# Optimization experiments

Hardware: AMD Instinct MI355X
Metric: run time of the kernel (lower is better)

## Reference

```python
import jax, jax.numpy as jnp
import numpy as np

N, T, D, H, P = 4096, 365, 16, 256, 2


def setup_inputs() -> dict:
    key = jax.random.key(0)
    ks = jax.random.split(key, 16)
    std = 0.02
    inputs = jax.random.normal(ks[0], (N, T, D), dtype=jnp.float32)
    A = jax.random.uniform(ks[1], (N, N), dtype=jnp.float32)
    A = A / jnp.sum(A, axis=1, keepdims=True)  # row-normalized adjacency
    return {
        "inputs": inputs,
        "A": A,
        # Keras LSTMCell params: kernel [D,4H], recurrent_kernel [H,4H], bias [4H]
        "kernel": jax.random.normal(ks[2], (D, 4 * H), dtype=jnp.float32) * std,
        "rkernel": jax.random.normal(ks[3], (H, 4 * H), dtype=jnp.float32) * std,
        "lstm_bias": jnp.zeros((4 * H,), dtype=jnp.float32),
        "W_graph_h": jax.random.normal(ks[4], (H, H), dtype=jnp.float32) * std,
        "b_graph_h": jnp.zeros((H,), dtype=jnp.float32),
        "W_graph_c": jax.random.normal(ks[5], (H, H), dtype=jnp.float32) * std,
        "b_graph_c": jnp.zeros((H,), dtype=jnp.float32),
        "W_h_cur": jax.random.normal(ks[6], (H, H), dtype=jnp.float32) * std,
        "W_h_prev": jax.random.normal(ks[7], (H, H), dtype=jnp.float32) * std,
        "b_h": jnp.zeros((H,), dtype=jnp.float32),
        "W_c_cur": jax.random.normal(ks[8], (H, H), dtype=jnp.float32) * std,
        "W_c_prev": jax.random.normal(ks[9], (H, H), dtype=jnp.float32) * std,
        "b_c": jnp.zeros((H,), dtype=jnp.float32),
        "W_out": jax.random.normal(ks[10], (H, P), dtype=jnp.float32) * std,
        "b_out": jnp.zeros((P,), dtype=jnp.float32),
    }


def reference(inputs, A, kernel, rkernel, lstm_bias,
              W_graph_h, b_graph_h, W_graph_c, b_graph_c,
              W_h_cur, W_h_prev, b_h, W_c_cur, W_c_prev, b_c,
              W_out, b_out):
    h = A.shape[0] and None  # noop; shapes: inputs [N,T,D]
    n = A.shape[0]
    hs = W_graph_h.shape[0]

    def step(carry, x_t):
        h_prev, c_prev = carry  # [N,H] each
        # graph propagation of previous states
        h_graph = jnp.tanh(A @ (h_prev @ W_graph_h + b_graph_h))
        c_graph = jnp.tanh(A @ (c_prev @ W_graph_c + b_graph_c))
        # Keras LSTMCell (gate order i, f, g, o)
        z = x_t @ kernel + h_prev @ rkernel + lstm_bias  # [N,4H]
        zi, zf, zg, zo = jnp.split(z, 4, axis=-1)
        c_cur = jax.nn.sigmoid(zf) * c_prev + jax.nn.sigmoid(zi) * jnp.tanh(zg)
        h_cur = jax.nn.sigmoid(zo) * jnp.tanh(c_cur)
        # gated merge of LSTM state and graph-propagated state
        h_update = jax.nn.sigmoid(h_cur @ W_h_cur + h_graph @ W_h_prev + b_h)
        c_update = jax.nn.sigmoid(c_cur @ W_c_cur + c_graph @ W_c_prev + b_c)
        out_pred = h_update @ W_out + b_out  # [N,P]
        return (h_update, c_update), out_pred

    init = (jnp.zeros((n, hs), dtype=inputs.dtype),
            jnp.zeros((n, hs), dtype=inputs.dtype))
    xs = jnp.swapaxes(inputs, 0, 1)  # [T,N,D]
    _, outs = jax.lax.scan(step, init, xs)  # [T,N,P]
    return jnp.swapaxes(outs, 0, 1)  # [N,T,P]
```

## Files before the change

### kernel.cpp

```cpp
#include <hip/hip_runtime.h>

using short8 = __attribute__((ext_vector_type(8))) short;
using f32x4  = __attribute__((ext_vector_type(4))) float;

#define NN 4096
#define TT 365
#define DD 16
#define HH 256
#define PP 2
#define TD (TT*DD)
#define TP (TT*PP)
#define KG 320
#define ASCALE 4096.0f
#define HWSCALE 64.0f
#define AINV2 (1.0f/(4096.0f*64.0f))

__device__ __forceinline__ unsigned short f2bf(float f) {
    union { float f; unsigned u; } v; v.f = f;
    unsigned r = v.u + 0x7FFFu + ((v.u >> 16) & 1u);
    return (unsigned short)(r >> 16);
}
__device__ __forceinline__ unsigned char f2e4m3(float f) {
    union { float f; unsigned u; } v; v.f = f;
    unsigned s = (v.u >> 24) & 0x80u;
    unsigned au = v.u & 0x7fffffffu;
    if (au >= 0x43E00000u) return (unsigned char)(s | 0x7E);
    if (au < 0x3C800000u) {
        int m = __float2int_rn(__uint_as_float(au) * 512.0f);
        return (unsigned char)(s | (unsigned)m);
    }
    unsigned r = au + 0x7FFFFu + ((au >> 20) & 1u);
    return (unsigned char)(s | ((r >> 20) - 0x3C0u));
}
__device__ __forceinline__ float sigmoidf_(float x) {
    return 1.0f / (1.0f + __expf(-x));
}
__device__ __forceinline__ float tanhf_(float x) {
    float t = __expf(2.0f * x);
    return (t - 1.0f) / (t + 1.0f);
}
__device__ __forceinline__ void async16(const void* g, void* l) {
    __builtin_amdgcn_global_load_lds(
        (const __attribute__((address_space(1))) void*)g,
        (__attribute__((address_space(3))) void*)l, 16, 0, 0);
}

template<int TI>
__device__ __forceinline__ void gemm_core_db(
    const unsigned short* __restrict__ Amat, int lda,
    const unsigned short* __restrict__ Bt,  int ldb,
    int k_len, int row0, int col0,
    unsigned short* As, unsigned short* Bs,
    f32x4 (&acc)[TI][4])
{
    const int tid  = threadIdx.x;
    const int lane = tid & 63;
    const int wave = tid >> 6;
    const int srow = lane >> 3;
    const int sblk = lane & 7;
    const int ABUF = TI * 32 * 64;
    const int BBUF = 128 * 64;

    const unsigned short* Ag = Amat + (size_t)(row0 + wave*8 + srow) * lda
                                    + ((sblk ^ srow) * 8);
    const unsigned short* Bg = Bt   + (size_t)(col0 + wave*8 + srow) * ldb
                                    + ((sblk ^ srow) * 8);

    const int fr = lane & 15;
    const int fq = lane >> 4;
    const int wr = (wave >> 1) * (TI * 16);
    const int wc = (wave & 1) * 64;
    const int off0 = ((fq ^ (fr & 7)) * 8);

    {
        unsigned short* AsW = As + wave * 512;
        unsigned short* BsW = Bs + wave * 512;
        #pragma unroll
        for (int q = 0; q < TI; q++) async16(Ag + (size_t)q * 32 * lda, AsW + q * 2048);
        #pragma unroll
        for (int q = 0; q < 4;  q++) async16(Bg + (size_t)q * 32 * ldb, BsW + q * 2048);
    }

    const int nk = k_len >> 6;
    int sel = 0;
    for (int it = 0; it < nk; ++it) {
        if (it + 1 < nk) {
            const unsigned short* Agn = Ag + (it + 1) * 64;
            const unsigned short* Bgn = Bg + (it + 1) * 64;
            unsigned short* AsW = As + (sel ^ 1) * ABUF + wave * 512;
            unsigned short* BsW = Bs + (sel ^ 1) * BBUF + wave * 512;
            #pragma unroll
            for (int q = 0; q < TI; q++) async16(Agn + (size_t)q * 32 * lda, AsW + q * 2048);
            #pragma unroll
            for (int q = 0; q < 4;  q++) async16(Bgn + (size_t)q * 32 * ldb, BsW + q * 2048);
            if constexpr (TI == 4)      asm volatile("s_waitcnt vmcnt(8)" ::: "memory");
            else if constexpr (TI == 2) asm volatile("s_waitcnt vmcnt(6)" ::: "memory");
            else                        asm volatile("s_waitcnt vmcnt(0)" ::: "memory");
        } else {
            asm volatile("s_waitcnt vmcnt(0)" ::: "memory");
        }
        __builtin_amdgcn_s_barrier();
        __builtin_amdgcn_sched_barrier(0);
        const unsigned short* Ab = As + sel * ABUF;
        const unsigned short* Bb = Bs + sel * BBUF;
        #pragma unroll
        for (int kh = 0; kh < 2; kh++) {
            const int off = off0 ^ (kh * 32);
            short8 a[TI], b[4];
            #pragma unroll
            for (int i = 0; i < TI; i++)
                a[i] = *(const short8*)(Ab + (wr + i*16 + fr) * 64 + off);
            #pragma unroll
            for (int j = 0; j < 4;  j++)
                b[j] = *(const short8*)(Bb + (wc + j*16 + fr) * 64 + off);
            #pragma unroll
            for (int i = 0; i < TI; i++)
                #pragma unroll
                for (int j = 0; j < 4; j++)
                    acc[i][j] = __builtin_amdgcn_mfma_f32_16x16x32_bf16(
                        a[i], b[j], acc[i][j], 0, 0, 0);
        }
        __builtin_amdgcn_s_barrier();
        sel ^= 1;
    }
}

template<int TI>
__device__ __forceinline__ void gemm8_db(
    const unsigned char* __restrict__ Amat,
    const unsigned char* __restrict__ Bmat,
    int kb, int klen, int row0, int col0,
    unsigned char* As, unsigned char* Bs,
    f32x4 (&acc)[TI][4])
{
    const int tid  = threadIdx.x;
    const int lane = tid & 63;
    const int wave = tid >> 6;
    const int srow = lane >> 3;
    const int sblk = lane & 7;
    const int ABUF = TI * 32 * 128;
    const int BBUF = 128 * 128;

    const unsigned char* Ag = Amat + (size_t)(row0 + wave*8 + srow) * NN
                                   + ((sblk ^ srow) * 16) + kb;
    const unsigned char* Bg = Bmat + (size_t)(col0 + wave*8 + srow) * NN
                                   + ((sblk ^ srow) * 16) + kb;

    const int fr = lane & 15;
    const int fq = lane >> 4;
    const int wr = (wave >> 1) * (TI * 16);
    const int wc = (wave & 1) * 64;
    int offk[4];
    #pragma unroll
    for (int kq = 0; kq < 4; kq++)
        offk[kq] = (((kq*2 + (fq >> 1)) ^ (fr & 7)) << 4) + ((fq & 1) << 3);

    {
        unsigned char* AsW = As + wave * 1024;
        unsigned char* BsW = Bs + wave * 1024;
        #pragma unroll
        for (int q = 0; q < TI; q++) async16(Ag + (size_t)q * 32 * NN, AsW + q * 4096);
        #pragma unroll
        for (int q = 0; q < 4;  q++) async16(Bg + (size_t)q * 32 * NN, BsW + q * 4096);
    }

    const int nk = klen >> 7;
    int sel = 0;
    for (int it = 0; it < nk; ++it) {
        if (it + 1 < nk) {
            const unsigned char* Agn = Ag + (size_t)(it + 1) * 128;
            const unsigned char* Bgn = Bg + (size_t)(it + 1) * 128;
            unsigned char* AsW = As + (sel ^ 1) * ABUF + wave * 1024;
            unsigned char* BsW = Bs + (sel ^ 1) * BBUF + wave * 1024;
            #pragma unroll
            for (int q = 0; q < TI; q++) async16(Agn + (size_t)q * 32 * NN, AsW + q * 4096);
            #pragma unroll
            for (int q = 0; q < 4;  q++) async16(Bgn + (size_t)q * 32 * NN, BsW + q * 4096);
            if constexpr (TI == 4)      asm volatile("s_waitcnt vmcnt(8)" ::: "memory");
            else if constexpr (TI == 2) asm volatile("s_waitcnt vmcnt(6)" ::: "memory");
            else                        asm volatile("s_waitcnt vmcnt(0)" ::: "memory");
        } else {
            asm volatile("s_waitcnt vmcnt(0)" ::: "memory");
        }
        __builtin_amdgcn_s_barrier();
        __builtin_amdgcn_sched_barrier(0);
        const unsigned char* Ab = As + sel * ABUF;
        const unsigned char* Bb = Bs + sel * BBUF;
        #pragma unroll
        for (int kq = 0; kq < 4; kq++) {
            long a[TI], b[4];
            #pragma unroll
            for (int i = 0; i < TI; i++) a[i] = *(const long*)(Ab + (wr + i*16 + fr) * 128 + offk[kq]);
            #pragma unroll
            for (int j = 0; j < 4;  j++) b[j] = *(const long*)(Bb + (wc + j*16 + fr) * 128 + offk[kq]);
            #pragma unroll
            for (int i = 0; i < TI; i++)
                #pragma unroll
                for (int j = 0; j < 4; j++)
                    acc[i][j] = __builtin_amdgcn_mfma_f32_16x16x32_fp8_fp8(
                        a[i], b[j], acc[i][j], 0, 0, 0);
        }
        __builtin_amdgcn_s_barrier();
        sel ^= 1;
    }
}


__global__ __launch_bounds__(256) void k_prep_a(const float* __restrict__ A,
                                                unsigned char* __restrict__ A8) {
    size_t i = (size_t)blockIdx.x * blockDim.x + threadIdx.x;
    size_t stride = (size_t)gridDim.x * blockDim.x;
    size_t total = (size_t)NN * NN / 4;
    for (; i < total; i += stride) {
        float4 v = ((const float4*)A)[i];
        unsigned pk = (unsigned)f2e4m3(v.x * ASCALE)
                    | ((unsigned)f2e4m3(v.y * ASCALE) << 8)
                    | ((unsigned)f2e4m3(v.z * ASCALE) << 16)
                    | ((unsigned)f2e4m3(v.w * ASCALE) << 24);
        ((unsigned*)A8)[i] = pk;
    }
}

__global__ __launch_bounds__(256) void k_prep_w(
    const float* __restrict__ Wgh, const float* __restrict__ Wgc,
    const float* __restrict__ rk,  const float* __restrict__ kern,
    const float* __restrict__ lb,
    const float* __restrict__ Whc, const float* __restrict__ Whp,
    const float* __restrict__ Wcc, const float* __restrict__ Wcp,
    unsigned short* __restrict__ WzTb, unsigned short* __restrict__ WgT,
    unsigned short* __restrict__ WU, float* __restrict__ biasg)
{
    int i = blockIdx.x * blockDim.x + threadIdx.x;
    int stride = gridDim.x * blockDim.x;
    for (int x = i; x < 1024 * KG; x += stride) {
        int col = x / KG, k = x % KG;
        int oc = (((col >> 4) & 3) << 8) + ((col >> 6) << 4) + (col & 15);
        float val = 0.f;
        if (k < 256) val = rk[k * 1024 + oc];
        else if (k < 272) val = kern[(k - 256) * 1024 + oc];
        WzTb[x] = f2bf(val);
    }
    for (int x = i; x < 512 * 256; x += stride) {
        int col = x >> 8, k = x & 255;
        float val = (col < 256) ? Wgh[k * 256 + col] : Wgc[k * 256 + (col - 256)];
        WgT[x] = f2bf(val);
    }
    for (int x = i; x < 512 * 512; x += stride) {
        int col = x >> 9, k = x & 511;
        float val;
        if (col < 256)
            val = (k < 256) ? Whc[k * 256 + col] : Whp[(k - 256) * 256 + col];
        else {
            int c2 = col - 256;
            val = (k < 256) ? Wcc[k * 256 + c2] : Wcp[(k - 256) * 256 + c2];
        }
        WU[x] = f2bf(val);
    }
    for (int x = i; x < 1024; x += stride)
        biasg[x] = lb[(((x >> 4) & 3) << 8) + ((x >> 6) << 4) + (x & 15)];
}

__global__ __launch_bounds__(256) void k_prep_s(const float* __restrict__ inputs,
                                                unsigned short* __restrict__ HCb,
                                                unsigned char* __restrict__ hwT8,
                                                float* __restrict__ Cstate)
{
    int i = blockIdx.x * blockDim.x + threadIdx.x;
    int stride = gridDim.x * blockDim.x;
    for (int x = i; x < NN * KG; x += stride) {
        int n = x / KG, col = x % KG;
        unsigned short v = 0;
        if (col >= 256 && col < 272)
            v = f2bf(inputs[(size_t)n * TD + (col - 256)]);
        HCb[x] = v;
    }
    for (int x = i; x < 512 * NN / 4; x += stride) ((unsigned*)hwT8)[x] = 0;
    for (int x = i; x < NN * HH; x += stride) Cstate[x] = 0.f;
}


__global__ __launch_bounds__(256, 2) void k_a(
    const unsigned char* __restrict__ A8,
    const unsigned char* __restrict__ hwT8,
    const float* __restrict__ bgh, const float* __restrict__ bgc,
    const unsigned short* __restrict__ HCb,
    const unsigned short* __restrict__ WzTb,
    const float* __restrict__ biasg,
    const float* __restrict__ Cstate,
    unsigned short* __restrict__ LHS3)
{
    __shared__ __align__(16) unsigned char smem[65536];
    const int bid = blockIdx.x;
    const int tid = threadIdx.x;
    const int lane = tid & 63;
    const int wave = tid >> 6;
    const int fr = lane & 15;
    const int rq = (lane >> 4) * 4;

    if (bid < 256) {
        const int x  = bid & 7;
        const int q  = bid >> 3;
        const int row0 = (x * 8 + (q & 7)) * 64;
        const int col0 = (q >> 3) * 128;
        f32x4 acc[2][4] = {};
        gemm8_db<2>(A8, hwT8, 0, NN, row0, col0, smem, smem + 16384, acc);
        const int wr = (wave >> 1) * 32;
        const int wc = (wave & 1) * 64;
        #pragma unroll
        for (int i = 0; i < 2; i++)
            #pragma unroll
            for (int j = 0; j < 4; j++) {
                int c = col0 + wc + j * 16 + fr;
                float bias = (c < 256) ? bgh[c] : bgc[c - 256];
                int dst = (c < 256) ? (c + 256) : (c + 512);
                int rbase = row0 + wr + i * 16 + rq;
                #pragma unroll
                for (int r = 0; r < 4; r++)
                    LHS3[(size_t)(rbase + r) * 1024 + dst] =
                        f2bf(tanhf_(acc[i][j][r] * AINV2 + bias));
            }
    } else {
        const int b2 = bid - 256;
        f32x4 acc[4][4] = {};
        const int row0 = (b2 >> 3) * 128;
        const int col0 = (b2 & 7) * 128;
        gemm_core_db<4>(HCb, KG, WzTb, KG, KG, row0, col0,
                        (unsigned short*)smem, (unsigned short*)(smem + 32768), acc);
        const int wr = (wave >> 1) * 64, wc = (wave & 1) * 64;
        const int h = (((col0 + wc) >> 6) << 4) + fr;
        float bgv[4];
        #pragma unroll
        for (int j = 0; j < 4; j++) bgv[j] = biasg[col0 + wc + j * 16 + fr];
        #pragma unroll
        for (int i = 0; i < 4; i++) {
            const int rbase = row0 + wr + i * 16 + rq;
            #pragma unroll
            for (int r = 0; r < 4; r++) {
                const int n = rbase + r;
                float z_i = acc[i][0][r] + bgv[0];
                float z_f = acc[i][1][r] + bgv[1];
                float z_g = acc[i][2][r] + bgv[2];
                float z_o = acc[i][3][r] + bgv[3];
                float cp = Cstate[n * HH + h];
                float ccur = sigmoidf_(z_f) * cp + sigmoidf_(z_i) * tanhf_(z_g);
                float hcur = sigmoidf_(z_o) * tanhf_(ccur);
                LHS3[(size_t)n * 1024 + h] = f2bf(hcur);
                LHS3[(size_t)n * 1024 + 512 + h] = f2bf(ccur);
            }
        }
    }
}

__global__ __launch_bounds__(256, 2) void k_uf(
    const unsigned short* __restrict__ LHS3,
    const unsigned short* __restrict__ WU,
    const unsigned short* __restrict__ WgT,
    const float* __restrict__ b_h, const float* __restrict__ b_c,
    const float* __restrict__ W_out, const float* __restrict__ b_out,
    float* __restrict__ Cstate,
    unsigned short* __restrict__ HCb,
    unsigned char* __restrict__ hwT8,
    float* __restrict__ d_out,
    const float* __restrict__ inputs, int t)
{
    __shared__ __align__(16) unsigned char smem[74752];
    unsigned short* As  = (unsigned short*)smem;
    unsigned short* Bs  = (unsigned short*)(smem + 8192);
    unsigned short* Us  = (unsigned short*)smem;
    unsigned short* B2s = (unsigned short*)(smem + 8192);
    float* outred = (float*)(smem + 73728);

    const int bid  = blockIdx.x;
    const int tid  = threadIdx.x;
    const int lane = tid & 63;
    const int wave = tid >> 6;
    const int fr   = lane & 15;
    const int fq   = lane >> 4;
    const int rq   = fq * 4;
    const int srow = lane >> 3;
    const int sblk = lane & 7;

    const int half = bid & 1;
    const int row0 = (bid >> 1) * 16;
    const int wc   = wave * 64;
    const int off0 = ((fq ^ (fr & 7)) * 8);
    const int ABUF = 1024, BBUF = 16384;

    const unsigned short* Ag = LHS3 + half*512
        + (size_t)(row0 + wave*8 + srow) * 1024 + ((sblk ^ srow) * 8);
    const unsigned short* Bg = WU
        + (size_t)(half*256 + wave*64 + srow) * 512 + ((sblk ^ srow) * 8);

    if (wave < 2) async16(Ag, As + wave*512);
    #pragma unroll
    for (int q = 0; q < 8; q++)
        async16(Bg + (size_t)q*8*512, Bs + wave*4096 + q*512);

    f32x4 acc[4] = {};
    int sel = 0;
    for (int it = 0; it < 8; ++it) {
        const int nit = it + 1;
        if (nit < 8) {
            if (wave < 2) async16(Ag + nit*64, As + (sel^1)*ABUF + wave*512);
            #pragma unroll
            for (int q = 0; q < 8; q++)
                async16(Bg + nit*64 + (size_t)q*8*512,
                        Bs + (sel^1)*BBUF + wave*4096 + q*512);
            if (wave < 2) asm volatile("s_waitcnt vmcnt(9)" ::: "memory");
            else          asm volatile("s_waitcnt vmcnt(8)" ::: "memory");
        } else {
            asm volatile("s_waitcnt vmcnt(0)" ::: "memory");
        }
        __builtin_amdgcn_s_barrier();
        __builtin_amdgcn_sched_barrier(0);
        const unsigned short* Ab = As + sel*ABUF;
        const unsigned short* Bb = Bs + sel*BBUF;
        #pragma unroll
        for (int kh2 = 0; kh2 < 2; kh2++) {
            const int off = off0 ^ (kh2 * 32);
            short8 a = *(const short8*)(Ab + fr * 64 + off);
            short8 b[4];
            #pragma unroll
            for (int j = 0; j < 4; j++)
                b[j] = *(const short8*)(Bb + (wc + j*16 + fr) * 64 + off);
            #pragma unroll
            for (int j = 0; j < 4; j++)
                acc[j] = __builtin_amdgcn_mfma_f32_16x16x32_bf16(
                    a, b[j], acc[j], 0, 0, 0);
        }
        __builtin_amdgcn_s_barrier();
        sel ^= 1;
    }

    const float* bias = half ? b_c : b_h;
    float pr0[4], pr1[4];
    #pragma unroll
    for (int m = 0; m < 4; m++) { pr0[m] = 0.f; pr1[m] = 0.f; }
    #pragma unroll
    for (int j = 0; j < 4; j++) {
        const int cl = wc + j*16 + fr;
        const float bv = bias[cl];
        const int blk = j*2 + (fr >> 3);
        float w0 = 0.f, w1 = 0.f;
        if (half == 0) { w0 = W_out[cl*2 + 0]; w1 = W_out[cl*2 + 1]; }
        #pragma unroll
        for (int r = 0; r < 4; r++) {
            const int rl = rq + r;
            const int n = row0 + rl;
            float v = sigmoidf_(acc[j][r] + bv);
            unsigned short vb = f2bf(v);
            Us[rl*256 + wave*64 + ((blk ^ (rl & 7)) * 8) + (fr & 7)] = vb;
            if (half == 0) {
                HCb[(size_t)n * KG + cl] = vb;
                pr0[r] += v * w0;
                pr1[r] += v * w1;
            } else {
                Cstate[(size_t)n * HH + cl] = v;
            }
        }
    }
    if (half == 0) {
        #pragma unroll
        for (int m = 0; m < 4; m++) {
            #pragma unroll
            for (int s = 1; s < 16; s <<= 1) {
                pr0[m] += __shfl_xor(pr0[m], s, 64);
                pr1[m] += __shfl_xor(pr1[m], s, 64);
            }
        }
        if (fr == 0) {
            #pragma unroll
            for (int r = 0; r < 4; r++) {
                int rl = rq + r;
                outred[(wave*16 + rl)*2 + 0] = pr0[r];
                outred[(wave*16 + rl)*2 + 1] = pr1[r];
            }
        }
    }
    __syncthreads();
    if (half == 0 && tid < 32) {
        int rl = tid >> 1, p = tid & 1;
        float s = b_out[p];
        #pragma unroll
        for (int w = 0; w < 4; w++) s += outred[(w*16 + rl)*2 + p];
        d_out[(size_t)(row0 + rl) * TP + t * PP + p] = s;
    }

    f32x4 acc2[4] = {};
    const unsigned short* Bg2 = WgT
        + (size_t)(half*256 + wave*64 + srow) * 256 + ((sblk ^ srow) * 8);
    #pragma unroll
    for (int q = 0; q < 8; q++)
        async16(Bg2 + (size_t)q*8*256, B2s + wave*4096 + q*512);
    int sel2 = 0;
    for (int kc2 = 0; kc2 < 4; ++kc2) {
        if (kc2 + 1 < 4) {
            #pragma unroll
            for (int q = 0; q < 8; q++)
                async16(Bg2 + (size_t)q*8*256 + (kc2+1)*64,
                        B2s + (sel2^1)*BBUF + wave*4096 + q*512);
            asm volatile("s_waitcnt vmcnt(8)" ::: "memory");
        } else {
            asm volatile("s_waitcnt vmcnt(0)" ::: "memory");
        }
        __builtin_amdgcn_s_barrier();
        __builtin_amdgcn_sched_barrier(0);
        const unsigned short* Bb2 = B2s + sel2*BBUF;
        #pragma unroll
        for (int kh2 = 0; kh2 < 2; kh2++) {
            const int off = off0 ^ (kh2 * 32);
            short8 a = *(const short8*)(Us + fr * 256 + kc2*64 + off);
            short8 b[4];
            #pragma unroll
            for (int j = 0; j < 4; j++)
                b[j] = *(const short8*)(Bb2 + (wc + j*16 + fr) * 64 + off);
            #pragma unroll
            for (int j = 0; j < 4; j++)
                acc2[j] = __builtin_amdgcn_mfma_f32_16x16x32_bf16(
                    a, b[j], acc2[j], 0, 0, 0);
        }
        __builtin_amdgcn_s_barrier();
        sel2 ^= 1;
    }
    unsigned pk[4];
    #pragma unroll
    for (int j = 0; j < 4; j++)
        pk[j] = (unsigned)f2e4m3(acc2[j][0] * HWSCALE)
              | ((unsigned)f2e4m3(acc2[j][1] * HWSCALE) << 8)
              | ((unsigned)f2e4m3(acc2[j][2] * HWSCALE) << 16)
              | ((unsigned)f2e4m3(acc2[j][3] * HWSCALE) << 24);
    unsigned o0 = 0, o1 = 0, o2 = 0, o3 = 0;
    #pragma unroll
    for (int d = 0; d < 4; d++) {
        unsigned g0 = __shfl(pk[d],  0 + fr, 64);
        unsigned g1 = __shfl(pk[d], 16 + fr, 64);
        unsigned g2 = __shfl(pk[d], 32 + fr, 64);
        unsigned g3 = __shfl(pk[d], 48 + fr, 64);
        if (fq == d) { o0 = g0; o1 = g1; o2 = g2; o3 = g3; }
    }
    {
        int cg = half*256 + wc + fq*16 + fr;
        uint4 o; o.x = o0; o.y = o1; o.z = o2; o.w = o3;
        *(uint4*)(hwT8 + (size_t)cg * NN + row0) = o;
    }

    if (half == 0 && t + 1 < TT) {
        int gid = (bid >> 1) * 256 + tid;
        int n = gid >> 4, d = gid & 15;
        HCb[(size_t)n * KG + 256 + d] = f2bf(inputs[(size_t)n * TD + (t + 1) * DD + d]);
    }
}

extern "C" void kernel_launch(void* const* d_in, const int* in_sizes, int n_in,
                              void* d_out_v, int out_size, void* d_ws, size_t ws_size,
                              hipStream_t stream)
{
    const float* inputs = (const float*)d_in[0];
    const float* A      = (const float*)d_in[1];
    const float* kern   = (const float*)d_in[2];
    const float* rk     = (const float*)d_in[3];
    const float* lb     = (const float*)d_in[4];
    const float* Wgh    = (const float*)d_in[5];
    const float* bgh    = (const float*)d_in[6];
    const float* Wgc    = (const float*)d_in[7];
    const float* bgc    = (const float*)d_in[8];
    const float* Whc    = (const float*)d_in[9];
    const float* Whp    = (const float*)d_in[10];
    const float* bh     = (const float*)d_in[11];
    const float* Wcc    = (const float*)d_in[12];
    const float* Wcp    = (const float*)d_in[13];
    const float* bc     = (const float*)d_in[14];
    const float* Wout   = (const float*)d_in[15];
    const float* bout   = (const float*)d_in[16];
    float* d_out = (float*)d_out_v;

    char* ws = (char*)d_ws;
    size_t off = 0;
    auto alloc = [&](size_t bytes) {
        char* p = ws + off;
        off += (bytes + 255) & ~(size_t)255;
        return p;
    };
    unsigned char*  A8    = (unsigned char*) alloc((size_t)NN * NN);
    unsigned char*  hwT8  = (unsigned char*) alloc((size_t)512 * NN);
    unsigned short* HCb   = (unsigned short*)alloc((size_t)NN * KG * 2);
    unsigned short* WzTb  = (unsigned short*)alloc((size_t)1024 * KG * 2);
    unsigned short* WgT   = (unsigned short*)alloc((size_t)512 * 256 * 2);
    unsigned short* WU    = (unsigned short*)alloc((size_t)512 * 512 * 2);
    float*          biasg = (float*)         alloc(1024 * 4);
    unsigned short* LHS3  = (unsigned short*)alloc((size_t)NN * 1024 * 2);
    float*          Cst   = (float*)         alloc((size_t)NN * HH * 4);
    (void)in_sizes; (void)n_in; (void)out_size; (void)ws_size;

    k_prep_a<<<2048, 256, 0, stream>>>(A, A8);
    k_prep_w<<<256, 256, 0, stream>>>(Wgh, Wgc, rk, kern, lb,
                                      Whc, Whp, Wcc, Wcp, WzTb, WgT, WU, biasg);
    k_prep_s<<<512, 256, 0, stream>>>(inputs, HCb, hwT8, Cst);

    for (int t = 0; t < TT; t++) {
        k_a<<<512, 256, 0, stream>>>(A8, hwT8, bgh, bgc,
                                     HCb, WzTb, biasg, Cst, LHS3);
        k_uf<<<512, 256, 0, stream>>>(LHS3, WU, WgT, bh, bc, Wout, bout,
                                      Cst, HCb, hwT8, d_out, inputs, t);
    }
}
```

Measured before the change: 15.49 ms.

## Load k_uf GEMM operands directly from global, drop LDS staging

```diff
diff --git a/kernel.cpp b/kernel.cpp
--- a/kernel.cpp
+++ b/kernel.cpp
@@ -351,7 +351,7 @@
     }
 }
 
-__global__ __launch_bounds__(256, 2) void k_uf(
+__global__ __launch_bounds__(256, 4) void k_uf(
     const unsigned short* __restrict__ LHS3,
     const unsigned short* __restrict__ WU,
     const unsigned short* __restrict__ WgT,
@@ -363,12 +363,9 @@
     float* __restrict__ d_out,
     const float* __restrict__ inputs, int t)
 {
-    __shared__ __align__(16) unsigned char smem[74752];
-    unsigned short* As  = (unsigned short*)smem;
-    unsigned short* Bs  = (unsigned short*)(smem + 8192);
-    unsigned short* Us  = (unsigned short*)smem;
-    unsigned short* B2s = (unsigned short*)(smem + 8192);
-    float* outred = (float*)(smem + 73728);
+    __shared__ __align__(16) unsigned char smem[8704];
+    unsigned short* Us = (unsigned short*)smem;
+    float* outred = (float*)(smem + 8192);
 
     const int bid  = blockIdx.x;
     const int tid  = threadIdx.x;
@@ -377,59 +374,34 @@
     const int fr   = lane & 15;
     const int fq   = lane >> 4;
     const int rq   = fq * 4;
-    const int srow = lane >> 3;
-    const int sblk = lane & 7;
 
     const int half = bid & 1;
     const int row0 = (bid >> 1) * 16;
     const int wc   = wave * 64;
     const int off0 = ((fq ^ (fr & 7)) * 8);
-    const int ABUF = 1024, BBUF = 16384;
-
-    const unsigned short* Ag = LHS3 + half*512
-        + (size_t)(row0 + wave*8 + srow) * 1024 + ((sblk ^ srow) * 8);
-    const unsigned short* Bg = WU
-        + (size_t)(half*256 + wave*64 + srow) * 512 + ((sblk ^ srow) * 8);
-
-    if (wave < 2) async16(Ag, As + wave*512);
-    #pragma unroll
-    for (int q = 0; q < 8; q++)
-        async16(Bg + (size_t)q*8*512, Bs + wave*4096 + q*512);
+
+    const unsigned short* Arow = LHS3 + (size_t)(row0 + fr) * 1024 + half*512 + fq*8;
+    const unsigned short* Brow[4];
+    #pragma unroll
+    for (int j = 0; j < 4; j++)
+        Brow[j] = WU + (size_t)(half*256 + wc + j*16 + fr) * 512 + fq*8;
 
     f32x4 acc[4] = {};
-    int sel = 0;
+    #pragma unroll
     for (int it = 0; it < 8; ++it) {
-        const int nit = it + 1;
-        if (nit < 8) {
-            if (wave < 2) async16(Ag + nit*64, As + (sel^1)*ABUF + wave*512);
-            #pragma unroll
-            for (int q = 0; q < 8; q++)
-                async16(Bg + nit*64 + (size_t)q*8*512,
-                        Bs + (sel^1)*BBUF + wave*4096 + q*512);
-            if (wave < 2) asm volatile("s_waitcnt vmcnt(9)" ::: "memory");
-            else          asm volatile("s_waitcnt vmcnt(8)" ::: "memory");
-        } else {
-            asm volatile("s_waitcnt vmcnt(0)" ::: "memory");
-        }
-        __builtin_amdgcn_s_barrier();
-        __builtin_amdgcn_sched_barrier(0);
-        const unsigned short* Ab = As + sel*ABUF;
-        const unsigned short* Bb = Bs + sel*BBUF;
         #pragma unroll
         for (int kh2 = 0; kh2 < 2; kh2++) {
-            const int off = off0 ^ (kh2 * 32);
-            short8 a = *(const short8*)(Ab + fr * 64 + off);
+            const int ko = it*64 + kh2*32;
+            short8 a = *(const short8*)(Arow + ko);
             short8 b[4];
             #pragma unroll
             for (int j = 0; j < 4; j++)
-                b[j] = *(const short8*)(Bb + (wc + j*16 + fr) * 64 + off);
+                b[j] = *(const short8*)(Brow[j] + ko);
             #pragma unroll
             for (int j = 0; j < 4; j++)
                 acc[j] = __builtin_amdgcn_mfma_f32_16x16x32_bf16(
                     a, b[j], acc[j], 0, 0, 0);
         }
-        __builtin_amdgcn_s_barrier();
-        sel ^= 1;
     }
 
     const float* bias = half ? b_c : b_h;
@@ -487,40 +459,26 @@
     }
 
     f32x4 acc2[4] = {};
-    const unsigned short* Bg2 = WgT
-        + (size_t)(half*256 + wave*64 + srow) * 256 + ((sblk ^ srow) * 8);
-    #pragma unroll
-    for (int q = 0; q < 8; q++)
-        async16(Bg2 + (size_t)q*8*256, B2s + wave*4096 + q*512);
-    int sel2 = 0;
+    const unsigned short* B2row[4];
+    #pragma unroll
+    for (int j = 0; j < 4; j++)
+        B2row[j] = WgT + (size_t)(half*256 + wc + j*16 + fr) * 256 + fq*8;
+    #pragma unroll
     for (int kc2 = 0; kc2 < 4; ++kc2) {
-        if (kc2 + 1 < 4) {
-            #pragma unroll
-            for (int q = 0; q < 8; q++)
-                async16(Bg2 + (size_t)q*8*256 + (kc2+1)*64,
-                        B2s + (sel2^1)*BBUF + wave*4096 + q*512);
-            asm volatile("s_waitcnt vmcnt(8)" ::: "memory");
-        } else {
-            asm volatile("s_waitcnt vmcnt(0)" ::: "memory");
-        }
-        __builtin_amdgcn_s_barrier();
-        __builtin_amdgcn_sched_barrier(0);
-        const unsigned short* Bb2 = B2s + sel2*BBUF;
         #pragma unroll
         for (int kh2 = 0; kh2 < 2; kh2++) {
             const int off = off0 ^ (kh2 * 32);
+            const int ko = kc2*64 + kh2*32;
             short8 a = *(const short8*)(Us + fr * 256 + kc2*64 + off);
             short8 b[4];
             #pragma unroll
             for (int j = 0; j < 4; j++)
-                b[j] = *(const short8*)(Bb2 + (wc + j*16 + fr) * 64 + off);
+                b[j] = *(const short8*)(B2row[j] + ko);
             #pragma unroll
             for (int j = 0; j < 4; j++)
                 acc2[j] = __builtin_amdgcn_mfma_f32_16x16x32_bf16(
                     a, b[j], acc2[j], 0, 0, 0);
         }
-        __builtin_amdgcn_s_barrier();
-        sel2 ^= 1;
     }
     unsigned pk[4];
     #pragma unroll
```

Result: slower. 21.76 ms (+40.4%).
